# Kernel tuning notes

Hardware: AMD Instinct MI355X
Metric: run time of the kernel (lower is better)

The kernel has to match this reference:

```python
import jax, jax.numpy as jnp
import numpy as np

B, S, D_MODEL, D_K, D_V = 8, 2048, 1024, 1024, 1024


def setup_inputs() -> dict:
    key = jax.random.key(0)
    ks = jax.random.split(key, 10)
    scale = 1.0 / np.sqrt(D_MODEL)
    return {
        "inputs_q": jax.random.normal(ks[0], (B, S, D_MODEL), dtype=jnp.float32),
        "inputs_k": jax.random.normal(ks[1], (B, S, D_MODEL), dtype=jnp.float32),
        "inputs_v": jax.random.normal(ks[2], (B, S, D_MODEL), dtype=jnp.float32),
        "mask": jax.random.randint(ks[3], (B, S), 0, 2, dtype=jnp.int32),
        "Wq": jax.random.normal(ks[4], (D_MODEL, D_K), dtype=jnp.float32) * scale,
        "bq": jnp.zeros((D_K,), dtype=jnp.float32),
        "Wk": jax.random.normal(ks[5], (D_MODEL, D_K), dtype=jnp.float32) * scale,
        "bk": jnp.zeros((D_K,), dtype=jnp.float32),
        "Wv": jax.random.normal(ks[6], (D_MODEL, D_V), dtype=jnp.float32) * scale,
        "bv": jnp.zeros((D_V,), dtype=jnp.float32),
    }


def reference(inputs_q, inputs_k, inputs_v, mask, Wq, bq, Wk, bk, Wv, bv):
    # Dense projections: [B,S,d_model] @ [d_model,d] + bias
    q = jnp.einsum("bsd,dk->bsk", inputs_q, Wq) + bq
    k = jnp.einsum("bsd,dk->bsk", inputs_k, Wk) + bk
    v = jnp.einsum("bsd,dv->bsv", inputs_v, Wv) + bv
    # scaled dot-product scores [B,S,S]
    scores = jnp.einsum("bqk,bsk->bqs", q, k) / jnp.sqrt(jnp.float32(D_K))
    # padding mask [B,S] -> matrix mask via min(row, col); 1 = valid
    m = mask.astype(jnp.float32)
    matrix_mask = jnp.minimum(m[:, :, None], m[:, None, :])  # [B,S,S]
    mask_float = 1.0 - matrix_mask  # 1 where masked
    scores = scores + mask_float * (-1e9)
    attention_weights = jax.nn.softmax(scores, axis=-1)
    out = jnp.einsum("bqs,bsv->bqv", attention_weights, v)  # [B,S,d_v]
    return out
```

## Files before the change

kernel.cpp:

```cpp
#include <hip/hip_runtime.h>
#include <stdint.h>


typedef unsigned short u16;
typedef __attribute__((ext_vector_type(8))) short short8;
typedef __attribute__((ext_vector_type(4))) float f32x4;

__device__ __forceinline__ u16 f2bf(float x) {
  unsigned u = __float_as_uint(x);
  return (u16)((u + 0x7FFFu + ((u >> 16) & 1u)) >> 16);
}
__device__ __forceinline__ float bf2f(u16 h) {
  return __uint_as_float(((unsigned)h) << 16);
}

__device__ __forceinline__ void stage16(const void* g, void* l) {
  const __attribute__((address_space(1))) uint32_t* gp =
      (const __attribute__((address_space(1))) uint32_t*)(uintptr_t)g;
  __attribute__((address_space(3))) uint32_t* lp =
      (__attribute__((address_space(3))) uint32_t*)(uintptr_t)l;
  __builtin_amdgcn_global_load_lds(gp, lp, 16, 0, 0);
}

__device__ __forceinline__ short8 ld8(const char* p, int off) {
  return *(const short8*)(p + off);
}

__global__ __launch_bounds__(256) void maskscan(const int* __restrict__ mask,
                                                int* __restrict__ idxA,
                                                int* __restrict__ nvA,
                                                int* __restrict__ nvpadA) {
  const int b = blockIdx.x;
  const int t = threadIdx.x, lane = t & 63, w = t >> 6;
  const int* m = mask + b * 2048;
  int v[8], loc = 0;
#pragma unroll
  for (int i = 0; i < 8; ++i) { v[i] = m[t * 8 + i]; loc += v[i]; }
  int sc = loc;
  for (int off = 1; off < 64; off <<= 1) {
    int n = __shfl_up(sc, off);
    if (lane >= off) sc += n;
  }
  __shared__ int wsum[4];
  if (lane == 63) wsum[w] = sc;
  __syncthreads();
  int woff = 0;
  for (int i = 0; i < w; ++i) woff += wsum[i];
  int pos = woff + sc - loc;
#pragma unroll
  for (int i = 0; i < 8; ++i)
    if (v[i]) idxA[b * 2048 + (pos++)] = t * 8 + i;
  if (t == 255) {
    const int nv = woff + sc;
    nvA[b] = nv;
    nvpadA[b] = (nv + 255) & ~255;
  }
}

__global__ __launch_bounds__(256) void compact3(const float* __restrict__ Xq,
                                                const float* __restrict__ Xk,
                                                const float* __restrict__ Xv,
                                                const int* __restrict__ idxA,
                                                const int* __restrict__ nvA,
                                                u16* __restrict__ Oq,
                                                u16* __restrict__ Ok,
                                                u16* __restrict__ Ov) {
  const int b = blockIdx.y, j = blockIdx.x, z = blockIdx.z;
  if (j >= nvA[b]) return;
  const float* X = (z == 0) ? Xq : (z == 1) ? Xk : Xv;
  u16* out = (z == 0) ? Oq : (z == 1) ? Ok : Ov;
  const int src = idxA[b * 2048 + j];
  const float4* s = (const float4*)(X + ((size_t)b * 2048 + src) * 1024);
  ushort4* d = (ushort4*)(out + ((size_t)b * 2048 + j) * 1024);
  const float4 f = s[threadIdx.x];
  ushort4 o;
  o.x = f2bf(f.x); o.y = f2bf(f.y); o.z = f2bf(f.z); o.w = f2bf(f.w);
  d[threadIdx.x] = o;
}

__global__ __launch_bounds__(256) void colpart(const float* __restrict__ X,
                                               float* __restrict__ partial) {
  const int b = blockIdx.x, dq = blockIdx.y, sck = blockIdx.z;
  const int d = dq * 256 + threadIdx.x;
  const float* p = X + ((size_t)b * 2048 + sck * 256) * 1024 + d;
  float s0 = 0, s1 = 0, s2 = 0, s3 = 0;
  for (int r = 0; r < 256; r += 4) {
    s0 += p[(size_t)(r + 0) * 1024];
    s1 += p[(size_t)(r + 1) * 1024];
    s2 += p[(size_t)(r + 2) * 1024];
    s3 += p[(size_t)(r + 3) * 1024];
  }
  partial[((size_t)b * 8 + sck) * 1024 + d] = (s0 + s1) + (s2 + s3);
}

__global__ __launch_bounds__(256) void vpartk(const float* __restrict__ partial,
                                              const float* __restrict__ Wv,
                                              float* __restrict__ vpart) {
  const int b = blockIdx.x, cq = blockIdx.y, dk = blockIdx.z;
  const int t = threadIdx.x;
  __shared__ float mx[128];
  if (t < 128) {
    const int d = dk * 128 + t;
    float m = 0;
#pragma unroll
    for (int i = 0; i < 8; ++i) m += partial[((size_t)b * 8 + i) * 1024 + d];
    mx[t] = m * (1.0f / 2048.0f);
  }
  __syncthreads();
  const int c = cq * 256 + t;
  const float* wp = Wv + (size_t)(dk * 128) * 1024 + c;
  float acc = 0;
#pragma unroll 4
  for (int i = 0; i < 128; ++i) acc += mx[i] * wp[(size_t)i * 1024];
  vpart[((size_t)b * 8 + dk) * 1024 + c] = acc;
}

__global__ __launch_bounds__(256) void vmeanred(const float* __restrict__ vpart,
                                                const float* __restrict__ bv,
                                                float* __restrict__ vmean) {
  const int b = blockIdx.x;
  const int c = blockIdx.y * 256 + threadIdx.x;
  float acc = bv[c];
#pragma unroll
  for (int i = 0; i < 8; ++i) acc += vpart[((size_t)b * 8 + i) * 1024 + c];
  vmean[b * 1024 + c] = acc;
}

__global__ __launch_bounds__(256) void bcast(const int* __restrict__ mask,
                                             const float* __restrict__ vmean,
                                             float* __restrict__ out) {
  const int b = blockIdx.y, row = blockIdx.x;
  if (mask[b * 2048 + row] != 0) return;
  const float4 vv = ((const float4*)(vmean + b * 1024))[threadIdx.x];
  ((float4*)(out + ((size_t)b * 2048 + row) * 1024))[threadIdx.x] = vv;
}

__global__ __launch_bounds__(256) void wtrans3(const float* __restrict__ Wq,
                                               const float* __restrict__ Wk,
                                               const float* __restrict__ Wv,
                                               u16* __restrict__ WT) {
  __shared__ float tile[32][33];
  const int z = blockIdx.z;
  const float* W = (z == 0) ? Wq : (z == 1) ? Wk : Wv;
  u16* out = WT + (size_t)z * 1024 * 1024;
  const int tx = threadIdx.x, ty = threadIdx.y;
  const int d0 = blockIdx.y * 32, n0 = blockIdx.x * 32;
#pragma unroll
  for (int i = 0; i < 4; ++i)
    tile[ty + 8 * i][tx] = W[(size_t)(d0 + ty + 8 * i) * 1024 + n0 + tx];
  __syncthreads();
#pragma unroll
  for (int i = 0; i < 4; ++i)
    out[(size_t)(n0 + ty + 8 * i) * 1024 + d0 + tx] = f2bf(tile[tx][ty + 8 * i]);
}


#define BAR __builtin_amdgcn_s_barrier()

#define RDQ(DST, K0, K1, QOFF)                              \
  {                                                         \
    DST[0][0] = ld8(K0, (QOFF));                            \
    DST[0][1] = ld8(K0, (QOFF) + 2048);                     \
    DST[1][0] = ld8(K1, (QOFF));                            \
    DST[1][1] = ld8(K1, (QOFF) + 2048);                     \
  }

#define RDB(DST, K0, K1, NH)                                \
  {                                                         \
    DST[0][0] = ld8(K0, (NH) * 4096);                       \
    DST[0][1] = ld8(K0, (NH) * 4096 + 2048);                \
    DST[1][0] = ld8(K1, (NH) * 4096);                       \
    DST[1][1] = ld8(K1, (NH) * 4096 + 2048);                \
  }

#define MQ(ACC, MB, NH, A2, B2)                                          \
  __builtin_amdgcn_s_setprio(1);                                         \
  {                                                                      \
    _Pragma("unroll") for (int ks_ = 0; ks_ < 2; ++ks_)                  \
        _Pragma("unroll") for (int m_ = 0; m_ < 2; ++m_)                 \
            _Pragma("unroll") for (int nf_ = 0; nf_ < 2; ++nf_)          \
                ACC[(MB) + m_][(NH) * 2 + nf_] =                         \
                    __builtin_amdgcn_mfma_f32_16x16x32_bf16(             \
                        A2[ks_][m_], B2[ks_][nf_],                       \
                        ACC[(MB) + m_][(NH) * 2 + nf_], 0, 0, 0);        \
  }                                                                      \
  __builtin_amdgcn_s_setprio(0);

template <int MODE>
__global__ __launch_bounds__(512, 2) void gemm8p(
    const u16* __restrict__ A, const u16* __restrict__ B,
    void* __restrict__ C, void* __restrict__ C1, void* __restrict__ C2,
    const float* __restrict__ b0, const float* __restrict__ b1,
    const float* __restrict__ b2,
    const int* __restrict__ nvpadA, const int* __restrict__ nvA,
    const int* __restrict__ idxA,
    int K, int lda, int ldb, int ldc,
    size_t Az, size_t Bz, size_t Cz) {
  __shared__ __attribute__((aligned(16))) char smem[131072];
  const int tid = threadIdx.x;
  const int lane = tid & 63;
  const int w = tid >> 6;
  const int wr = w >> 2;
  const int wc = w & 3;

  const int bx = blockIdx.x;
  const int z = bx & 7;
  int r = bx >> 3;
  int bm, bn, o = 0;
  if constexpr (MODE == 0) { o = r >> 5; r &= 31; bm = r >> 2; bn = r & 3; }
  else if constexpr (MODE == 2) { bm = r >> 3; bn = r & 7; }
  else { bm = r >> 2; bn = r & 3; }

  const int nvp = nvpadA[z];
  if (bm * 256 >= nvp) return;
  if constexpr (MODE == 2) { if (bn * 256 >= nvp) return; }

  const u16* Ap = A;
  const u16* Bp = B;
  if constexpr (MODE == 0) {
    Ap += (size_t)o * (8u * 2048u * 1024u) + (size_t)z * (2048u * 1024u);
    Bp += (size_t)o * (1024u * 1024u);
  } else {
    Ap += (size_t)z * Az;
    Bp += (size_t)z * Bz;
  }
  const int Kz = (MODE == 3) ? nvp : K;
  const int half = Kz >> 7;

  const int srow = w * 8 + (lane >> 3);
  const int scol = ((lane & 7) ^ (lane >> 3)) << 3;
  const u16* Ab0 = Ap + (size_t)(bm * 256 + srow) * lda + scol;
  const u16* Ab1 = Ab0 + (size_t)64 * lda;
  const u16* Ab2 = Ab0 + (size_t)128 * lda;
  const u16* Ab3 = Ab0 + (size_t)192 * lda;
  const u16* Bb0 = Bp + (size_t)(bn * 256 + srow) * ldb + scol;
  const u16* Bb1 = Bb0 + (size_t)64 * ldb;
  const u16* Bb2 = Bb0 + (size_t)128 * ldb;
  const u16* Bb3 = Bb0 + (size_t)192 * ldb;
  char* ldsW = smem + w * 1024;

  const int fr = lane & 15;
  const int fq = lane >> 4;
  const int fx = (fr & 7) << 4;
  const char* pak0 = smem + wr * 16384 + fr * 128 + ((fq * 16) ^ fx);
  const char* pak1 = smem + wr * 16384 + fr * 128 + ((64 + fq * 16) ^ fx);
  const char* pak0b = pak0 + 65536;
  const char* pak1b = pak1 + 65536;
  const char* pbk0 = smem + 32768 + wc * 8192 + fr * 128 + ((fq * 16) ^ fx);
  const char* pbk1 = smem + 32768 + wc * 8192 + fr * 128 + ((64 + fq * 16) ^ fx);
  const char* pbk0b = pbk0 + 65536;
  const char* pbk1b = pbk1 + 65536;

  f32x4 acc0[4][4] = {};
  f32x4 acc1[4][4] = {};
  short8 aA[2][2], aB[2][2], bf0[2][2], bf1[2][2];

  stage16(Ab0, ldsW + 0);     stage16(Ab1, ldsW + 8192);
  stage16(Ab2, ldsW + 16384); stage16(Ab3, ldsW + 24576);
  stage16(Bb0, ldsW + 32768); stage16(Bb1, ldsW + 40960);
  stage16(Bb2, ldsW + 49152); stage16(Bb3, ldsW + 57344);
  stage16(Bb0 + 64, ldsW + 98304);  stage16(Bb1 + 64, ldsW + 106496);
  stage16(Bb2 + 64, ldsW + 114688); stage16(Bb3 + 64, ldsW + 122880);
  stage16(Ab0 + 64, ldsW + 65536);
  asm volatile("s_waitcnt vmcnt(5)" ::: "memory");
  BAR;
  RDQ(aA, pak0, pak1, 0);
  RDB(bf0, pbk0, pbk1, 0);

  int koff = 0;
  for (int i = 0; i < half; ++i) {
    const bool st = (i + 1 < half);
    const int o1 = koff + 64, o2 = koff + 128, o3 = koff + 192;

    RDB(bf1, pbk0, pbk1, 1);
    BAR;
    stage16(Ab1 + o1, ldsW + 65536 + 8192);
    MQ(acc0, 0, 0, aA, bf0);
    RDQ(aB, pak0, pak1, 4096);
    BAR;
    stage16(Ab2 + o1, ldsW + 65536 + 16384);
    MQ(acc0, 0, 1, aA, bf1);
    BAR;
    stage16(Ab3 + o1, ldsW + 65536 + 24576);
    MQ(acc0, 2, 0, aB, bf0);
    RDQ(aA, pak0, pak1, 8192);
    BAR;
    if (st) stage16(Bb0 + o2, ldsW + 32768);
    MQ(acc0, 2, 1, aB, bf1);
    BAR;
    if (st) stage16(Bb1 + o2, ldsW + 40960);
    MQ(acc1, 0, 0, aA, bf0);
    RDQ(aB, pak0, pak1, 12288);
    BAR;
    if (st) stage16(Bb2 + o2, ldsW + 49152);
    MQ(acc1, 0, 1, aA, bf1);
    BAR;
    if (st) stage16(Bb3 + o2, ldsW + 57344);
    MQ(acc1, 2, 0, aB, bf0);
    if (st) { asm volatile("s_waitcnt vmcnt(4)" ::: "memory"); }
    else    { asm volatile("s_waitcnt vmcnt(0)" ::: "memory"); }
    BAR;
    RDQ(aA, pak0b, pak1b, 0);
    RDB(bf0, pbk0b, pbk1b, 0);
    if (st) stage16(Ab0 + o2, ldsW + 0);
    MQ(acc1, 2, 1, aB, bf1);

    RDB(bf1, pbk0b, pbk1b, 1);
    BAR;
    if (st) stage16(Ab1 + o2, ldsW + 8192);
    MQ(acc0, 0, 0, aA, bf0);
    RDQ(aB, pak0b, pak1b, 4096);
    BAR;
    if (st) stage16(Ab2 + o2, ldsW + 16384);
    MQ(acc0, 0, 1, aA, bf1);
    BAR;
    if (st) stage16(Ab3 + o2, ldsW + 24576);
    MQ(acc0, 2, 0, aB, bf0);
    RDQ(aA, pak0b, pak1b, 8192);
    BAR;
    if (st) stage16(Bb0 + o3, ldsW + 98304);
    MQ(acc0, 2, 1, aB, bf1);
    BAR;
    if (st) stage16(Bb1 + o3, ldsW + 106496);
    MQ(acc1, 0, 0, aA, bf0);
    RDQ(aB, pak0b, pak1b, 12288);
    BAR;
    if (st) stage16(Bb2 + o3, ldsW + 114688);
    MQ(acc1, 0, 1, aA, bf1);
    BAR;
    if (st) stage16(Bb3 + o3, ldsW + 122880);
    MQ(acc1, 2, 0, aB, bf0);
    if (st) { asm volatile("s_waitcnt vmcnt(4)" ::: "memory"); }
    else    { asm volatile("s_waitcnt vmcnt(0)" ::: "memory"); }
    BAR;
    RDQ(aA, pak0, pak1, 0);
    RDB(bf0, pbk0, pbk1, 0);
    if (st) stage16(Ab0 + o3, ldsW + 65536);
    MQ(acc1, 2, 1, aB, bf1);

    koff += 128;
  }

  const int colb = bn * 256 + wc * 64 + fr;
#pragma unroll
  for (int mh = 0; mh < 2; ++mh) {
    f32x4(&ac)[4][4] = mh ? acc1 : acc0;
    const int rowl = bm * 256 + wr * 128 + mh * 64 + fq * 4;
    if constexpr (MODE == 0) {
      if (o < 2) {
        const float* bp = o ? b1 : b0;
        u16* Cb = (u16*)(o ? C1 : C) + (size_t)z * (2048u * 1024u);
#pragma unroll
        for (int mf = 0; mf < 4; ++mf)
#pragma unroll
          for (int n = 0; n < 4; ++n) {
            const int c = colb + n * 16;
            const float bv = bp[c];
#pragma unroll
            for (int j = 0; j < 4; ++j)
              Cb[(size_t)(rowl + mf * 16 + j) * 1024 + c] =
                  f2bf(ac[mf][n][j] + bv);
          }
      } else {
        u16* Cb = (u16*)C2;
#pragma unroll
        for (int mf = 0; mf < 4; ++mf) {
          const int s_ = rowl + mf * 16;
#pragma unroll
          for (int n = 0; n < 4; ++n) {
            const int c = colb + n * 16;
            const float bv = b2[c];
            ushort4 ov;
            ov.x = f2bf(ac[mf][n][0] + bv);
            ov.y = f2bf(ac[mf][n][1] + bv);
            ov.z = f2bf(ac[mf][n][2] + bv);
            ov.w = f2bf(ac[mf][n][3] + bv);
            *(ushort4*)&Cb[((size_t)z * 1024 + c) * 2048 + s_] = ov;
          }
        }
      }
    } else if constexpr (MODE == 2) {
      u16* Cb = (u16*)C + (size_t)z * Cz;
#pragma unroll
      for (int mf = 0; mf < 4; ++mf)
#pragma unroll
        for (int n = 0; n < 4; ++n) {
          const int c = colb + n * 16;
#pragma unroll
          for (int j = 0; j < 4; ++j)
            Cb[(size_t)(rowl + mf * 16 + j) * ldc + c] =
                f2bf(ac[mf][n][j] * 0.03125f);
        }
    } else {
      const int nv = nvA[z];
      const int* idxp = idxA + z * 2048;
      float* Ob = (float*)C;
#pragma unroll
      for (int mf = 0; mf < 4; ++mf)
#pragma unroll
        for (int j = 0; j < 4; ++j) {
          const int rowc = rowl + mf * 16 + j;
          if (rowc < nv) {
            const int gr = idxp[rowc];
            float* orow = Ob + ((size_t)z * 2048 + gr) * 1024;
#pragma unroll
            for (int n = 0; n < 4; ++n) orow[colb + n * 16] = ac[mf][n][j];
          }
        }
    }
  }
}

__global__ __launch_bounds__(256) void softmaxc(u16* __restrict__ scores,
                                                const int* __restrict__ nvA,
                                                const int* __restrict__ nvpadA) {
  const int b = blockIdx.y, row = blockIdx.x;
  const int nv = nvA[b];
  if (row >= nv) return;
  const int nvp = nvpadA[b];
  const int t = threadIdx.x, lane = t & 63, w = t >> 6;
  u16* sc = scores + ((size_t)b * 2048 + row) * 2048;
  const int c0 = t * 8;
  float v[8];
  if (c0 < nvp) {
    const ushort4 h0 = *(const ushort4*)&sc[c0];
    const ushort4 h1 = *(const ushort4*)&sc[c0 + 4];
    v[0] = bf2f(h0.x); v[1] = bf2f(h0.y); v[2] = bf2f(h0.z); v[3] = bf2f(h0.w);
    v[4] = bf2f(h1.x); v[5] = bf2f(h1.y); v[6] = bf2f(h1.z); v[7] = bf2f(h1.w);
  } else {
#pragma unroll
    for (int i = 0; i < 8; ++i) v[i] = 0.f;
  }
  float lmax = -3.0e38f;
#pragma unroll
  for (int i = 0; i < 8; ++i)
    if (c0 + i < nv) lmax = fmaxf(lmax, v[i]);
#pragma unroll
  for (int off = 32; off >= 1; off >>= 1) lmax = fmaxf(lmax, __shfl_xor(lmax, off));
  __shared__ float red[8];
  if (lane == 0) red[w] = lmax;
  __syncthreads();
  const float bmax = fmaxf(fmaxf(red[0], red[1]), fmaxf(red[2], red[3]));
  float e[8];
  float lsum = 0.f;
#pragma unroll
  for (int i = 0; i < 8; ++i) {
    e[i] = (c0 + i < nv) ? __expf(v[i] - bmax) : 0.f;
    lsum += e[i];
  }
#pragma unroll
  for (int off = 32; off >= 1; off >>= 1) lsum += __shfl_xor(lsum, off);
  if (lane == 0) red[4 + w] = lsum;
  __syncthreads();
  const float inv = 1.0f / ((red[4] + red[5]) + (red[6] + red[7]));
  if (c0 < nvp) {
    ushort4 o0, o1;
    o0.x = f2bf(e[0] * inv); o0.y = f2bf(e[1] * inv);
    o0.z = f2bf(e[2] * inv); o0.w = f2bf(e[3] * inv);
    o1.x = f2bf(e[4] * inv); o1.y = f2bf(e[5] * inv);
    o1.z = f2bf(e[6] * inv); o1.w = f2bf(e[7] * inv);
    *(ushort4*)&sc[c0] = o0;
    *(ushort4*)&sc[c0 + 4] = o1;
  }
}

extern "C" void kernel_launch(void* const* d_in, const int* in_sizes, int n_in,
                              void* d_out, int out_size, void* d_ws, size_t ws_size,
                              hipStream_t stream) {
  const float* in_q = (const float*)d_in[0];
  const float* in_k = (const float*)d_in[1];
  const float* in_v = (const float*)d_in[2];
  const int* mask = (const int*)d_in[3];
  const float* Wq = (const float*)d_in[4];
  const float* bq = (const float*)d_in[5];
  const float* Wk = (const float*)d_in[6];
  const float* bk = (const float*)d_in[7];
  const float* Wv = (const float*)d_in[8];
  const float* bv = (const float*)d_in[9];

  char* ws = (char*)d_ws;
  const size_t SZ = (size_t)16384 * 1024 * 2;
  u16* qc = (u16*)(ws);
  u16* kc = (u16*)(ws + SZ);
  u16* vcT = (u16*)(ws + 2 * SZ);
  u16* Xc = (u16*)(ws + 3 * SZ);
  u16* Xqc = Xc;
  u16* Xkc = Xc + (size_t)8 * 2048 * 1024;
  u16* Xvc = Xkc + (size_t)8 * 2048 * 1024;
  u16* scores = (u16*)(ws + 3 * SZ);
  u16* WT = (u16*)(ws + 6 * SZ);
  char* misc = ws + 6 * SZ + 6 * 1024 * 1024;
  int* idxA = (int*)misc;
  int* nvA = idxA + 8 * 2048;
  int* nvpadA = nvA + 8;
  float* partial = (float*)(misc + 128 * 1024);
  float* vmean = (float*)(misc + 384 * 1024);
  float* vpart = (float*)(misc + 448 * 1024);

  maskscan<<<8, 256, 0, stream>>>(mask, idxA, nvA, nvpadA);

  compact3<<<dim3(2048, 8, 3), 256, 0, stream>>>(in_q, in_k, in_v, idxA, nvA,
                                                 Xqc, Xkc, Xvc);
  colpart<<<dim3(8, 4, 8), 256, 0, stream>>>(in_v, partial);
  vpartk<<<dim3(8, 4, 8), 256, 0, stream>>>(partial, Wv, vpart);
  vmeanred<<<dim3(8, 4), 256, 0, stream>>>(vpart, bv, vmean);

  wtrans3<<<dim3(32, 32, 3), dim3(32, 8), 0, stream>>>(Wq, Wk, Wv, WT);

  gemm8p<0><<<768, 512, 0, stream>>>(
      Xqc, WT, qc, kc, vcT, bq, bk, bv, nvpadA, nvA, idxA,
      1024, 1024, 1024, 1024, 0, 0, 0);

  gemm8p<2><<<512, 512, 0, stream>>>(
      qc, kc, scores, nullptr, nullptr, nullptr, nullptr, nullptr,
      nvpadA, nvA, idxA, 1024, 1024, 1024, 2048,
      (size_t)2048 * 1024, (size_t)2048 * 1024, (size_t)2048 * 2048);

  softmaxc<<<dim3(2048, 8), 256, 0, stream>>>(scores, nvA, nvpadA);

  gemm8p<3><<<256, 512, 0, stream>>>(
      scores, vcT, d_out, nullptr, nullptr, nullptr, nullptr, nullptr,
      nvpadA, nvA, idxA, 0, 2048, 2048, 1024,
      (size_t)2048 * 2048, (size_t)1024 * 2048, 0);

  bcast<<<dim3(2048, 8), 256, 0, stream>>>(mask, vmean, (float*)d_out);
}
```

Measured before the change: 281.6 us.

## Restructure GEMM main loop into 8-phase schedule with explicit waits and peeled tail

Rewrites the inner K loop of the bf16 MFMA GEMM into eight phases, each loading four A fragments and two B fragments, issuing two global-to-LDS stages, then doing 16 MFMAs between barriers with explicit lgkmcnt/vmcnt waits and scheduling barriers. The last iteration is peeled so the per-stage conditionals go away. The aim is tighter interleaving of LDS reads, global prefetch and MFMA work, plus less branch overhead. In exchange it adds more barriers per iteration, and the wider A fragment set raises register pressure.

New measurement: 282.5 us. No clear change (+0.3%).

```diff
diff --git a/kernel.cpp b/kernel.cpp
--- a/kernel.cpp
+++ b/kernel.cpp
@@ -156,33 +156,37 @@
 
 
 #define BAR __builtin_amdgcn_s_barrier()
-
-#define RDQ(DST, K0, K1, QOFF)                              \
-  {                                                         \
-    DST[0][0] = ld8(K0, (QOFF));                            \
-    DST[0][1] = ld8(K0, (QOFF) + 2048);                     \
-    DST[1][0] = ld8(K1, (QOFF));                            \
-    DST[1][1] = ld8(K1, (QOFF) + 2048);                     \
-  }
-
-#define RDB(DST, K0, K1, NH)                                \
-  {                                                         \
-    DST[0][0] = ld8(K0, (NH) * 4096);                       \
-    DST[0][1] = ld8(K0, (NH) * 4096 + 2048);                \
-    DST[1][0] = ld8(K1, (NH) * 4096);                       \
-    DST[1][1] = ld8(K1, (NH) * 4096 + 2048);                \
-  }
-
-#define MQ(ACC, MB, NH, A2, B2)                                          \
+#define SB __builtin_amdgcn_sched_barrier(0)
+#define LGK0 asm volatile("s_waitcnt lgkmcnt(0)" ::: "memory")
+#define VM4 asm volatile("s_waitcnt vmcnt(4)" ::: "memory")
+#define VM0 asm volatile("s_waitcnt vmcnt(0)" ::: "memory")
+
+#define RDA4(P0, P1, MH)                                      \
+  {                                                           \
+    _Pragma("unroll") for (int mf_ = 0; mf_ < 4; ++mf_) {     \
+      afr[0][mf_] = ld8(P0, (MH) * 8192 + mf_ * 2048);        \
+      afr[1][mf_] = ld8(P1, (MH) * 8192 + mf_ * 2048);        \
+    }                                                         \
+  }
+
+#define RDB2(DST, P0, P1, NH)                                 \
+  {                                                           \
+    DST[0][0] = ld8(P0, (NH) * 4096);                         \
+    DST[0][1] = ld8(P0, (NH) * 4096 + 2048);                  \
+    DST[1][0] = ld8(P1, (NH) * 4096);                         \
+    DST[1][1] = ld8(P1, (NH) * 4096 + 2048);                  \
+  }
+
+#define MQ16(ACC, NH, BF)                                                \
   __builtin_amdgcn_s_setprio(1);                                         \
   {                                                                      \
     _Pragma("unroll") for (int ks_ = 0; ks_ < 2; ++ks_)                  \
-        _Pragma("unroll") for (int m_ = 0; m_ < 2; ++m_)                 \
+        _Pragma("unroll") for (int mf_ = 0; mf_ < 4; ++mf_)              \
             _Pragma("unroll") for (int nf_ = 0; nf_ < 2; ++nf_)          \
-                ACC[(MB) + m_][(NH) * 2 + nf_] =                         \
+                ACC[mf_][(NH) * 2 + nf_] =                               \
                     __builtin_amdgcn_mfma_f32_16x16x32_bf16(             \
-                        A2[ks_][m_], B2[ks_][nf_],                       \
-                        ACC[(MB) + m_][(NH) * 2 + nf_], 0, 0, 0);        \
+                        afr[ks_][mf_], BF[ks_][nf_],                     \
+                        ACC[mf_][(NH) * 2 + nf_], 0, 0, 0);              \
   }                                                                      \
   __builtin_amdgcn_s_setprio(0);
 
@@ -253,92 +257,62 @@
 
   f32x4 acc0[4][4] = {};
   f32x4 acc1[4][4] = {};
-  short8 aA[2][2], aB[2][2], bf0[2][2], bf1[2][2];
-
+  short8 afr[2][4], bf0[2][2], bf1[2][2];
+
+  stage16(Bb0, ldsW + 32768); stage16(Bb1, ldsW + 40960);
+  stage16(Bb2, ldsW + 49152); stage16(Bb3, ldsW + 57344);
   stage16(Ab0, ldsW + 0);     stage16(Ab1, ldsW + 8192);
   stage16(Ab2, ldsW + 16384); stage16(Ab3, ldsW + 24576);
-  stage16(Bb0, ldsW + 32768); stage16(Bb1, ldsW + 40960);
-  stage16(Bb2, ldsW + 49152); stage16(Bb3, ldsW + 57344);
   stage16(Bb0 + 64, ldsW + 98304);  stage16(Bb1 + 64, ldsW + 106496);
   stage16(Bb2 + 64, ldsW + 114688); stage16(Bb3 + 64, ldsW + 122880);
-  stage16(Ab0 + 64, ldsW + 65536);
-  asm volatile("s_waitcnt vmcnt(5)" ::: "memory");
+  VM4;
   BAR;
-  RDQ(aA, pak0, pak1, 0);
-  RDB(bf0, pbk0, pbk1, 0);
 
   int koff = 0;
-  for (int i = 0; i < half; ++i) {
-    const bool st = (i + 1 < half);
+  for (int i = 0; i < half - 1; ++i) {
     const int o1 = koff + 64, o2 = koff + 128, o3 = koff + 192;
-
-    RDB(bf1, pbk0, pbk1, 1);
-    BAR;
-    stage16(Ab1 + o1, ldsW + 65536 + 8192);
-    MQ(acc0, 0, 0, aA, bf0);
-    RDQ(aB, pak0, pak1, 4096);
-    BAR;
-    stage16(Ab2 + o1, ldsW + 65536 + 16384);
-    MQ(acc0, 0, 1, aA, bf1);
-    BAR;
-    stage16(Ab3 + o1, ldsW + 65536 + 24576);
-    MQ(acc0, 2, 0, aB, bf0);
-    RDQ(aA, pak0, pak1, 8192);
-    BAR;
-    if (st) stage16(Bb0 + o2, ldsW + 32768);
-    MQ(acc0, 2, 1, aB, bf1);
-    BAR;
-    if (st) stage16(Bb1 + o2, ldsW + 40960);
-    MQ(acc1, 0, 0, aA, bf0);
-    RDQ(aB, pak0, pak1, 12288);
-    BAR;
-    if (st) stage16(Bb2 + o2, ldsW + 49152);
-    MQ(acc1, 0, 1, aA, bf1);
-    BAR;
-    if (st) stage16(Bb3 + o2, ldsW + 57344);
-    MQ(acc1, 2, 0, aB, bf0);
-    if (st) { asm volatile("s_waitcnt vmcnt(4)" ::: "memory"); }
-    else    { asm volatile("s_waitcnt vmcnt(0)" ::: "memory"); }
-    BAR;
-    RDQ(aA, pak0b, pak1b, 0);
-    RDB(bf0, pbk0b, pbk1b, 0);
-    if (st) stage16(Ab0 + o2, ldsW + 0);
-    MQ(acc1, 2, 1, aB, bf1);
-
-    RDB(bf1, pbk0b, pbk1b, 1);
-    BAR;
-    if (st) stage16(Ab1 + o2, ldsW + 8192);
-    MQ(acc0, 0, 0, aA, bf0);
-    RDQ(aB, pak0b, pak1b, 4096);
-    BAR;
-    if (st) stage16(Ab2 + o2, ldsW + 16384);
-    MQ(acc0, 0, 1, aA, bf1);
-    BAR;
-    if (st) stage16(Ab3 + o2, ldsW + 24576);
-    MQ(acc0, 2, 0, aB, bf0);
-    RDQ(aA, pak0b, pak1b, 8192);
-    BAR;
-    if (st) stage16(Bb0 + o3, ldsW + 98304);
-    MQ(acc0, 2, 1, aB, bf1);
-    BAR;
-    if (st) stage16(Bb1 + o3, ldsW + 106496);
-    MQ(acc1, 0, 0, aA, bf0);
-    RDQ(aB, pak0b, pak1b, 12288);
-    BAR;
-    if (st) stage16(Bb2 + o3, ldsW + 114688);
-    MQ(acc1, 0, 1, aA, bf1);
-    BAR;
-    if (st) stage16(Bb3 + o3, ldsW + 122880);
-    MQ(acc1, 2, 0, aB, bf0);
-    if (st) { asm volatile("s_waitcnt vmcnt(4)" ::: "memory"); }
-    else    { asm volatile("s_waitcnt vmcnt(0)" ::: "memory"); }
-    BAR;
-    RDQ(aA, pak0, pak1, 0);
-    RDB(bf0, pbk0, pbk1, 0);
-    if (st) stage16(Ab0 + o3, ldsW + 65536);
-    MQ(acc1, 2, 1, aB, bf1);
-
+    RDA4(pak0, pak1, 0); RDB2(bf0, pbk0, pbk1, 0);
+    stage16(Ab0 + o1, ldsW + 65536); stage16(Ab1 + o1, ldsW + 73728);
+    SB; BAR; LGK0; MQ16(acc0, 0, bf0); BAR;
+    RDB2(bf1, pbk0, pbk1, 1);
+    stage16(Ab2 + o1, ldsW + 81920); stage16(Ab3 + o1, ldsW + 90112);
+    SB; BAR; LGK0; MQ16(acc0, 1, bf1); BAR;
+    RDA4(pak0, pak1, 1);
+    stage16(Bb0 + o2, ldsW + 32768); stage16(Bb1 + o2, ldsW + 40960);
+    SB; BAR; LGK0; MQ16(acc1, 0, bf0); BAR;
+    stage16(Bb2 + o2, ldsW + 49152); stage16(Bb3 + o2, ldsW + 57344);
+    SB; BAR; MQ16(acc1, 1, bf1); VM4; BAR;
+    RDA4(pak0b, pak1b, 0); RDB2(bf0, pbk0b, pbk1b, 0);
+    stage16(Ab0 + o2, ldsW + 0); stage16(Ab1 + o2, ldsW + 8192);
+    SB; BAR; LGK0; MQ16(acc0, 0, bf0); BAR;
+    RDB2(bf1, pbk0b, pbk1b, 1);
+    stage16(Ab2 + o2, ldsW + 16384); stage16(Ab3 + o2, ldsW + 24576);
+    SB; BAR; LGK0; MQ16(acc0, 1, bf1); BAR;
+    RDA4(pak0b, pak1b, 1);
+    stage16(Bb0 + o3, ldsW + 98304); stage16(Bb1 + o3, ldsW + 106496);
+    SB; BAR; LGK0; MQ16(acc1, 0, bf0); BAR;
+    stage16(Bb2 + o3, ldsW + 114688); stage16(Bb3 + o3, ldsW + 122880);
+    SB; BAR; MQ16(acc1, 1, bf1); VM4; BAR;
     koff += 128;
+  }
+  {
+    const int o1 = koff + 64;
+    RDA4(pak0, pak1, 0); RDB2(bf0, pbk0, pbk1, 0);
+    stage16(Ab0 + o1, ldsW + 65536); stage16(Ab1 + o1, ldsW + 73728);
+    SB; BAR; LGK0; MQ16(acc0, 0, bf0); BAR;
+    RDB2(bf1, pbk0, pbk1, 1);
+    stage16(Ab2 + o1, ldsW + 81920); stage16(Ab3 + o1, ldsW + 90112);
+    SB; BAR; LGK0; MQ16(acc0, 1, bf1); BAR;
+    RDA4(pak0, pak1, 1);
+    SB; BAR; LGK0; MQ16(acc1, 0, bf0); BAR;
+    SB; BAR; MQ16(acc1, 1, bf1); VM0; BAR;
+    RDA4(pak0b, pak1b, 0); RDB2(bf0, pbk0b, pbk1b, 0);
+    SB; BAR; LGK0; MQ16(acc0, 0, bf0); BAR;
+    RDB2(bf1, pbk0b, pbk1b, 1);
+    SB; BAR; LGK0; MQ16(acc0, 1, bf1); BAR;
+    RDA4(pak0b, pak1b, 1);
+    SB; BAR; LGK0; MQ16(acc1, 0, bf0); BAR;
+    SB; BAR; MQ16(acc1, 1, bf1); BAR;
   }
 
   const int colb = bn * 256 + wc * 64 + fr;
```
